# Performance work log

Measured on AMD Instinct MI355X. Metric: run time of the kernel, lower is better.

## Reference

```python
import jax, jax.numpy as jnp
import numpy as np

B = 32          # batch of input networks (INRs)
D = 128         # d_hid
H = 8           # attention heads
DH = D // H
L = 3           # RT layers
DOUT = 10
LAYOUT = [2, 32, 32, 1]          # INR layer layout -> graph nodes
N = 2 + 32 + 32 + 1              # 67 nodes
POS_LAYOUT = [1, 1, 32, 32, 1]   # [1]*layout[0] + layout[1:-1] + [1]*layout[-1]


def _ln(x, g, b, eps=1e-5):
    m = x.mean(-1, keepdims=True)
    v = ((x - m) ** 2).mean(-1, keepdims=True)
    return (x - m) * jax.lax.rsqrt(v + eps) * g + b


def _gelu(x):
    return jax.nn.gelu(x, approximate=False)


def setup_inputs() -> dict:
    key = jax.random.key(0)
    cnt = [0]
    def nk():
        cnt[0] += 1
        return jax.random.fold_in(key, cnt[0])
    def rn(shape, s=0.02):
        return (s * jax.random.normal(nk(), shape)).astype(jnp.float32)
    z = lambda *s: jnp.zeros(s, jnp.float32)
    o = lambda *s: jnp.ones(s, jnp.float32)
    inp = dict(
        w0=rn((B, 2, 32, 1), 1.0), w1=rn((B, 32, 32, 1), 1.0), w2=rn((B, 32, 1, 1), 1.0),
        b0=rn((B, 32, 1), 1.0), b1=rn((B, 32, 1), 1.0), b2=rn((B, 1, 1), 1.0),
        pw_W=rn((1, D)), pw_b=z(D), pb_W=rn((1, D)), pb_b=z(D),
        node_in_W=rn((D, D)), node_in_b=z(D), edge_in_W=rn((D, D)), edge_in_b=z(D),
        pos_embed=rn((len(POS_LAYOUT), D), 1.0),
        aln_g=o(L, D), aln_b=z(L, D),
        Wqkv_n=rn((L, D, 3 * D)), Wqkv_e=rn((L, D, 3 * D)), Wao=rn((L, D, D)), bao=z(L, D),
        Wl0=rn((L, D, D)), bl0=z(L, D),
        nln_g=o(L, D), nln_b=z(L, D),
        nW1=rn((L, D, 2 * D)), nb1=z(L, 2 * D), nW2=rn((L, 2 * D, D)), nb2=z(L, D),
        eln_g=o(L, D), eln_b=z(L, D),
        We=rn((L, 2 * D, D)), be=z(L, D),
        Ws=rn((L, D, D)), bs=z(L, D), Wt=rn((L, D, D)), bt=z(L, D),
        Wer=rn((L, D, D)), Wec=rn((L, D, D)), We1=rn((L, D, D)), be1=z(L, D),
        Wel0=rn((L, D, D)), bel0=z(L, D),
        mln_g=o(L, D), mln_b=z(L, D),
        mW1=rn((L, D, 2 * D)), mb1=z(L, 2 * D), mW2=rn((L, 2 * D, D)), mb2=z(L, D),
        Wo1=rn((D, D)), bo1=z(D), Wo2=rn((D, DOUT)), bo2=z(DOUT),
    )
    return inp


def _forward(w0, w1, w2, b0, b1, b2, pw_W, pw_b, pb_W, pb_b, node_in_W, node_in_b,
             edge_in_W, edge_in_b, pos_embed, aln_g, aln_b, Wqkv_n, Wqkv_e, Wao, bao,
             Wl0, bl0, nln_g, nln_b, nW1, nb1, nW2, nb2, eln_g, eln_b, We, be, Ws, bs,
             Wt, bt, Wer, Wec, We1, be1, Wel0, bel0, mln_g, mln_b, mW1, mb1, mW2, mb2,
             Wo1, bo1, Wo2, bo2):
    # ---- GraphConstructor / batch_to_graphs (layout [2,32,32,1], offsets 0/2/34/66) ----
    nf = jnp.zeros((B, N, 1), w0.dtype)
    ef = jnp.zeros((B, N, N, 1), w0.dtype)
    ef = ef.at[:, 0:2, 2:34].set(w0).at[:, 2:34, 34:66].set(w1).at[:, 34:66, 66:67].set(w2)
    nf = nf.at[:, 2:34].set(b0).at[:, 34:66].set(b1).at[:, 66:67].set(b2)
    node = nf @ pb_W + pb_b            # proj_bias: Linear(1, D)
    edge = ef @ pw_W + pw_b            # proj_weight: Linear(1, D)
    node = node @ node_in_W + node_in_b
    edge = edge @ edge_in_W + edge_in_b
    pos = jnp.concatenate([jnp.broadcast_to(pos_embed[i], (n, D))
                           for i, n in enumerate(POS_LAYOUT)], axis=0)  # [N, D]
    node = node + pos

    scale = 1.0 / np.sqrt(DH)
    for l in range(L):
        # ---- RTAttention (edge-biased multi-head attention) ----
        h = _ln(node, aln_g[l], aln_b[l])
        qkv_n = (h @ Wqkv_n[l]).reshape(B, N, H, 3, DH).transpose(0, 2, 3, 1, 4)       # b H 3 n dh
        qn, kn, vn = qkv_n[:, :, 0], qkv_n[:, :, 1], qkv_n[:, :, 2]
        qkv_e = (edge @ Wqkv_e[l]).reshape(B, N, N, H, 3, DH).transpose(0, 3, 4, 1, 2, 5)  # b H 3 n m dh
        q = qn[:, :, :, None, :] + qkv_e[:, :, 0]
        k = kn[:, :, None, :, :] + qkv_e[:, :, 1]
        v = vn[:, :, None, :, :] + qkv_e[:, :, 2]
        att = jax.nn.softmax((q * k).sum(-1) * scale, axis=-1)                          # b H n m
        o = jnp.einsum('bhnm,bhnmd->bhnd', att, v).transpose(0, 2, 1, 3).reshape(B, N, D)
        node = node + ((o @ Wao[l] + bao[l]) @ Wl0[l] + bl0[l])
        node = node + (_gelu(_ln(node, nln_g[l], nln_b[l]) @ nW1[l] + nb1[l]) @ nW2[l] + nb2[l])
        # ---- Edge update (EdgeMLP with forward/reversed edges + node/row/col terms) ----
        en = _ln(edge, eln_g[l], eln_b[l])
        m = jnp.concatenate([en, en.transpose(0, 2, 1, 3)], axis=-1) @ We[l] + be[l]
        m = m + (node @ Ws[l] + bs[l])[:, :, None, :] + (node @ Wt[l] + bt[l])[:, None, :, :]
        m = m + en.mean(2, keepdims=True) @ Wer[l] + en.mean(1, keepdims=True) @ Wec[l]
        m = _gelu(m) @ We1[l] + be1[l]
        edge = edge + (m @ Wel0[l] + bel0[l])
        edge = edge + (_gelu(_ln(edge, mln_g[l], mln_b[l]) @ mW1[l] + mb1[l]) @ mW2[l] + mb2[l])

    g = node.mean(1)                                        # mean pooling over nodes
    return jax.nn.relu(g @ Wo1 + bo1) @ Wo2 + bo2           # [B, DOUT]


def reference(w0, w1, w2, b0, b1, b2, pw_W, pw_b, pb_W, pb_b, node_in_W, node_in_b,
              edge_in_W, edge_in_b, pos_embed, aln_g, aln_b, Wqkv_n, Wqkv_e, Wao, bao,
              Wl0, bl0, nln_g, nln_b, nW1, nb1, nW2, nb2, eln_g, eln_b, We, be, Ws, bs,
              Wt, bt, Wer, Wec, We1, be1, Wel0, bel0, mln_g, mln_b, mW1, mb1, mW2, mb2,
              Wo1, bo1, Wo2, bo2):
    return _forward(w0, w1, w2, b0, b1, b2, pw_W, pw_b, pb_W, pb_b, node_in_W, node_in_b,
                    edge_in_W, edge_in_b, pos_embed, aln_g, aln_b, Wqkv_n, Wqkv_e, Wao, bao,
                    Wl0, bl0, nln_g, nln_b, nW1, nb1, nW2, nb2, eln_g, eln_b, We, be, Ws, bs,
                    Wt, bt, Wer, Wec, We1, be1, Wel0, bel0, mln_g, mln_b, mW1, mb1, mW2, mb2,
                    Wo1, bo1, Wo2, bo2)
```

## Files before the change

### kernel.cpp

```cpp
#include <hip/hip_runtime.h>
#include <math.h>

constexpr int B_ = 32, N_ = 67, D_ = 128, H_ = 8, DH_ = 16, L_ = 3;
constexpr int NN_ = N_ * N_;
constexpr int RN_ = B_ * N_;
constexpr int RE_ = B_ * NN_;
constexpr int DOUT_ = 10;

typedef __attribute__((ext_vector_type(8))) short short8;
typedef __attribute__((ext_vector_type(4))) float f32x4;

__device__ __forceinline__ float gelu_f(float x) {
  return 0.5f * x * (1.f + erff(x * 0.70710678118654752f));
}
__device__ __forceinline__ ushort f2b(float x) {
  union { float f; unsigned u; } v; v.f = x;
  return (ushort)((v.u + 0x7FFFu + ((v.u >> 16) & 1u)) >> 16);
}
__device__ __forceinline__ float b2f(ushort u) {
  union { unsigned u; float f; } v; v.u = (unsigned)u << 16; return v.f;
}

__global__ void k_comb(const float* __restrict__ Wao, const float* __restrict__ bao,
                       const float* __restrict__ Wl0, const float* __restrict__ bl0,
// ... 79 lines not shown
  node[idx] = nf * vecs[d] + vecs[D_ + d] + pos[pr * D_ + d];
}

__global__ void k_init_edge(const float* __restrict__ w0, const float* __restrict__ w1,
                            const float* __restrict__ w2, const float* __restrict__ vecs,
                            ushort* __restrict__ edge) {
  int idx = blockIdx.x * blockDim.x + threadIdx.x;
  if (idx >= RE_ * D_) return;
  int r = idx >> 7, d = idx & 127;
  int b = r / NN_;
  int rem = r - b * NN_;
  int n = rem / N_, m = rem - n * N_;
  float ef = 0.f;
  if (n < 2)        { if (m >= 2 && m < 34)  ef = w0[(b * 2 + n) * 32 + (m - 2)]; }
  else if (n < 34)  { if (m >= 34 && m < 66) ef = w1[(b * 32 + (n - 2)) * 32 + (m - 34)]; }
  else if (n < 66)  { if (m == 66)           ef = w2[b * 32 + (n - 34)]; }
  edge[idx] = f2b(ef * vecs[2 * D_ + d] + vecs[3 * D_ + d]);
}

__global__ void k_ln(const float* __restrict__ in, float* __restrict__ out,
                     const float* __restrict__ g, const float* __restrict__ b, int R) {
  int row = blockIdx.x * 4 + (threadIdx.x >> 6);
  int lane = threadIdx.x & 63;
  if (row >= R) return;
  const float* x = in + (size_t)row * D_;
  float x0 = x[lane], x1 = x[lane + 64];
  float s = x0 + x1;
  for (int off = 32; off; off >>= 1) s += __shfl_xor(s, off);
  float mean = s * (1.f / 128.f);
  float d0 = x0 - mean, d1 = x1 - mean;
  float v = d0 * d0 + d1 * d1;
  for (int off = 32; off; off >>= 1) v += __shfl_xor(v, off);
  float rstd = rsqrtf(v * (1.f / 128.f) + 1e-5f);
  out[(size_t)row * D_ + lane]      = d0 * rstd * g[lane] + b[lane];
  out[(size_t)row * D_ + lane + 64] = d1 * rstd * g[lane + 64] + b[lane + 64];
}

template <int MODE>
__global__ __launch_bounds__(256) void k_gemm(const float* __restrict__ A, const float* __restrict__ W,
                                              const float* __restrict__ bias, float* __restrict__ out,
                                              int R, int K, int C, int ldw, int ldo) {
  __shared__ float As[16][68];
  __shared__ float Wsh[16][68];
  int r0 = blockIdx.x * 64, c0 = blockIdx.y * 64;
  int tid = threadIdx.x;
  int tr = tid >> 4, tc = tid & 15;
  float acc[4][4] = {};
  for (int kk = 0; kk < K; kk += 16) {
#pragma unroll
    for (int i = 0; i < 4; i++) {
      int lin = tid + i * 256;
      int r_in = lin >> 4, k_in = lin & 15;
      int r = r0 + r_in;
      As[k_in][r_in] = (r < R) ? A[(size_t)r * K + kk + k_in] : 0.f;
    }
#pragma unroll
    for (int i = 0; i < 4; i++) {
      int lin = tid + i * 256;
      int k_in = lin >> 6, c_in = lin & 63;
      int c = c0 + c_in;
      Wsh[k_in][c_in] = (c < C) ? W[(size_t)(kk + k_in) * ldw + c] : 0.f;
    }
    __syncthreads();
#pragma unroll
    for (int k = 0; k < 16; k++) {
      float4 a4 = *reinterpret_cast<const float4*>(&As[k][tr * 4]);
      float4 b4 = *reinterpret_cast<const float4*>(&Wsh[k][tc * 4]);
      float av[4] = {a4.x, a4.y, a4.z, a4.w};
      float bv[4] = {b4.x, b4.y, b4.z, b4.w};
#pragma unroll
      for (int i = 0; i < 4; i++)
#pragma unroll
        for (int j = 0; j < 4; j++) acc[i][j] += av[i] * bv[j];
    }
    __syncthreads();
  }
#pragma unroll
  for (int i = 0; i < 4; i++) {
    int r = r0 + tr * 4 + i;
    if (r >= R) continue;
#pragma unroll
    for (int j = 0; j < 4; j++) {
      int c = c0 + tc * 4 + j;
      if (c >= C) continue;
      float v = acc[i][j] + (bias ? bias[c] : 0.f);
      size_t o = (size_t)r * ldo + c;
      if (MODE == 0) out[o] = v;
      else if (MODE == 1) out[o] = gelu_f(v);
      else out[o] += v;
    }
  }
}

__global__ __launch_bounds__(256) void k_nvec(
    const float* __restrict__ node, const float* __restrict__ rmean, const float* __restrict__ cmean,
    const float* __restrict__ Ws, const float* __restrict__ Wer,
    const float* __restrict__ Wt, const float* __restrict__ Wec,
    const float* __restrict__ bs, const float* __restrict__ be, const float* __restrict__ bt,
    float* __restrict__ rvec, float* __restrict__ cvec) {
  __shared__ float Ash[16][68];
  __shared__ float Wsh[16][68];
  int which = blockIdx.z;
  const float* A2 = which ? cmean : rmean;
  const float* W1 = which ? Wt : Ws;
  const float* W2 = which ? Wec : Wer;
  float* out = which ? cvec : rvec;
  int r0 = blockIdx.x * 64, c0 = blockIdx.y * 64;
  int tid = threadIdx.x, tr = tid >> 4, tc = tid & 15;
  float acc[4][4] = {};
  for (int kk = 0; kk < 256; kk += 16) {
#pragma unroll
    for (int i = 0; i < 4; i++) {
      int lin = tid + i * 256;
      int r_in = lin >> 4, k_in = lin & 15;
      int r = r0 + r_in, k = kk + k_in;
      float v = 0.f;
      if (r < RN_) v = (k < 128) ? node[(size_t)r * 128 + k] : A2[(size_t)r * 128 + (k - 128)];
      Ash[k_in][r_in] = v;
    }
#pragma unroll
    for (int i = 0; i < 4; i++) {
      int lin = tid + i * 256;
      int k_in = lin >> 6, c_in = lin & 63;
      int k = kk + k_in, c = c0 + c_in;
      Wsh[k_in][c_in] = (k < 128) ? W1[(size_t)k * 128 + c] : W2[(size_t)(k - 128) * 128 + c];
    }
    __syncthreads();
#pragma unroll
    for (int k = 0; k < 16; k++) {
      float4 a4 = *reinterpret_cast<const float4*>(&Ash[k][tr * 4]);
      float4 b4 = *reinterpret_cast<const float4*>(&Wsh[k][tc * 4]);
      float av[4] = {a4.x, a4.y, a4.z, a4.w};
      float bv[4] = {b4.x, b4.y, b4.z, b4.w};
#pragma unroll
      for (int i = 0; i < 4; i++)
#pragma unroll
        for (int j = 0; j < 4; j++) acc[i][j] += av[i] * bv[j];
    }
    __syncthreads();
  }
#pragma unroll
  for (int i = 0; i < 4; i++) {
    int r = r0 + tr * 4 + i;
    if (r >= RN_) continue;
#pragma unroll
    for (int j = 0; j < 4; j++) {
      int c = c0 + tc * 4 + j;
      float bias = which ? bt[c] : (bs[c] + be[c]);
      out[(size_t)r * 128 + c] = acc[i][j] + bias;
    }
  }
}

__global__ __launch_bounds__(256, 3) void k_eattn(
    const ushort* __restrict__ edge, const float* __restrict__ qkvn,
    const ushort* __restrict__ wqf,
    const float* __restrict__ gE, const float* __restrict__ bE,
    float* __restrict__ stats, float* __restrict__ rmean,
    float* __restrict__ obuf) {
  __shared__ __align__(16) ushort ed[68 * 128];
  __shared__ __align__(16) ushort Eb[68 * 202];
  __shared__ float qn_s[384];
  __shared__ float sc[4][68];
  __shared__ float red[4][16][4];
  __shared__ float stmu[68], strs[68];
  int bn = blockIdx.x;
  int b = bn / N_;
  int tid = threadIdx.x;
  int w = tid >> 6, lane = tid & 63, lr = lane & 15, lk8 = (lane >> 4) * 8;
  int swz = (lr & 7) << 3;
  int rb = (lane >> 4) * 4;
  size_t ebase = (size_t)bn * N_ * 128;

  for (int i = 0; i < 5; i++) {
    int u = tid + i * 256;
    if (u < 67 * 16) {
      int row = u >> 4, k8 = (u & 15) * 8;
      short8 t = __builtin_nontemporal_load(
          reinterpret_cast<const short8*>(&edge[ebase + (size_t)row * 128 + k8]));
      *reinterpret_cast<short8*>(&ed[row * 128 + (k8 ^ ((row & 7) << 3))]) = t;
      float s = 0.f, q = 0.f;
#pragma unroll
      for (int j = 0; j < 8; j++) { float v = b2f((ushort)t[j]); s += v; q += v * v; }
      for (int o = 8; o; o >>= 1) { s += __shfl_xor(s, o); q += __shfl_xor(q, o); }
      if ((u & 15) == 0) {
        float mu = s * (1.f / 128.f);
        float rs = rsqrtf(q * (1.f / 128.f) - mu * mu + 1e-5f);
        stmu[row] = mu; strs[row] = rs;
        stats[2 * (size_t)(bn * N_ + row)] = mu;
        stats[2 * (size_t)(bn * N_ + row) + 1] = rs;
      }
    }
  }
  for (int i = tid; i < 384; i += 256) qn_s[i] = qkvn[(size_t)bn * 384 + i];
  __syncthreads();
  if (tid < 128) {
    float s = 0.f;
    for (int m = 0; m < 67; m++)
      s += (b2f(ed[m * 128 + (tid ^ ((m & 7) << 3))]) - stmu[m]) * strs[m];
    rmean[(size_t)bn * 128 + tid] = gE[tid] * (s * (1.f / 67.f)) + bE[tid];
  }

  for (int ch = 0; ch < 2; ch++) {
    int h0 = ch * 4;
    f32x4 acc[5][3] = {};
#pragma unroll
    for (int ks = 0; ks < 4; ks++) {
      int kof = ks * 32 + lk8;
      short8 af[5];
#pragma unroll
      for (int rf = 0; rf < 5; rf++)
        af[rf] = *reinterpret_cast<const short8*>(&ed[(rf * 16 + lr) * 128 + (kof ^ swz)]);
#pragma unroll
      for (int cl = 0; cl < 3; cl++) {
        short8 bf = *reinterpret_cast<const short8*>(
            &wqf[(size_t)(((ch * 12 + w * 3 + cl) * 4 + ks) * 64 + lane) * 8]);
#pragma unroll
        for (int rf = 0; rf < 5; rf++)
          acc[rf][cl] = __builtin_amdgcn_mfma_f32_16x16x32_bf16(af[rf], bf, acc[rf][cl], 0, 0, 0);
      }
    }
#pragma unroll
    for (int rf = 0; rf < 5; rf++)
#pragma unroll
      for (int cl = 0; cl < 3; cl++) {
        int colc = (w * 3 + cl) * 16 + lr;
#pragma unroll
        for (int rg = 0; rg < 4; rg++) {
          int er = rf * 16 + rb + rg;
          if (er < 67) Eb[er * 202 + colc] = f2b(acc[rf][cl][rg]);
        }
      }
    __syncthreads();
    for (int idx = tid; idx < 268; idx += 256) {
      int h2 = idx / 67, m = idx - h2 * 67;
      const ushort* e = &Eb[m * 202 + h2 * 48];
      const float* kn = &qkvn[(size_t)(b * N_ + m) * 384 + (h0 + h2) * 48 + 16];
      const float* qn = &qn_s[(h0 + h2) * 48];
      float s2 = 0.f;
#pragma unroll
      for (int d = 0; d < 16; d++)
        s2 += (qn[d] + b2f(e[d])) * (kn[d] + b2f(e[16 + d]));
      sc[h2][m] = s2 * 0.25f;
    }
    __syncthreads();
    {
      float v0 = (lane < 67) ? sc[w][lane] : -1e30f;
      float v1 = (lane < 3) ? sc[w][lane + 64] : -1e30f;
      float mx = fmaxf(v0, v1);
      for (int o = 32; o; o >>= 1) mx = fmaxf(mx, __shfl_xor(mx, o));
      float e0 = (lane < 67) ? expf(v0 - mx) : 0.f;
      float e1 = (lane < 3) ? expf(v1 - mx) : 0.f;
      float ss = e0 + e1;
      for (int o = 32; o; o >>= 1) ss += __shfl_xor(ss, o);
      float inv = 1.f / ss;
      if (lane < 67) sc[w][lane] = e0 * inv;
      if (lane < 3) sc[w][lane + 64] = e1 * inv;
    }
    __syncthreads();
    {
      int item = tid >> 2, c = tid & 3;
      int h2 = item >> 4, d = item & 15;
      float p = 0.f;
      for (int m = c; m < 67; m += 4) {
        float v = qkvn[(size_t)(b * N_ + m) * 384 + (h0 + h2) * 48 + 32 + d]
                + b2f(Eb[m * 202 + h2 * 48 + 32 + d]);
        p += sc[h2][m] * v;
      }
      red[h2][d][c] = p;
    }
    __syncthreads();
    if (tid < 64) {
      int h2 = tid >> 4, d = tid & 15;
      obuf[(size_t)bn * 128 + (h0 + h2) * 16 + d] =
          red[h2][d][0] + red[h2][d][1] + red[h2][d][2] + red[h2][d][3];
    }
    __syncthreads();
  }
}

__global__ void k_colmean(const ushort* __restrict__ edge, const float* __restrict__ stats,
                          const float* __restrict__ g, const float* __restrict__ bb,
                          float* __restrict__ cmean) {
  int bm = blockIdx.x;
  int b = bm / N_, m = bm - b * N_;
  int d = threadIdx.x;
  float s = 0.f;
  for (int n = 0; n < N_; n++) {
    size_t r = (size_t)b * NN_ + (size_t)n * N_ + m;
    s += (b2f(edge[r * D_ + d]) - stats[2 * r]) * stats[2 * r + 1];
  }
  cmean[(size_t)bm * D_ + d] = g[d] * (s * (1.f / 67.f)) + bb[d];
}

__global__ __launch_bounds__(256, 2) void k_fedge(
    const ushort* __restrict__ ein, ushort* __restrict__ eout,
    const float* __restrict__ stats,
    const float* __restrict__ gE, const float* __restrict__ bE,
    const ushort* __restrict__ wef,
    const float* __restrict__ rvec, const float* __restrict__ cvec,
    const ushort* __restrict__ wcef,
    const float* __restrict__ bcE,
    const float* __restrict__ gM, const float* __restrict__ bM,
    const ushort* __restrict__ w1f,
    const float* __restrict__ mb1,
    const ushort* __restrict__ w2f,
    const float* __restrict__ mb2) {
  __shared__ __align__(16) ushort As[64 * 256];
  __shared__ __align__(16) ushort mt[64 * 128];
  __shared__ __align__(16) ushort Wb[32 * 512];
  int tid = threadIdx.x;
  int r0 = blockIdx.x * 64;
  int w = tid >> 6, lane = tid & 63, lr = lane & 15, lk8 = (lane >> 4) * 8;
  int swz = (lr & 7) << 3;
  int rb = (lane >> 4) * 4;
  int arow = w * 16 + lr;

  auto stageW = [&](const ushort* src) {
#pragma unroll
    for (int i = 0; i < 8; i++) {
      int u = tid + i * 256;
      short8 t = *reinterpret_cast<const short8*>(&src[(size_t)u * 8]);
      *reinterpret_cast<short8*>(&Wb[u * 8]) = t;
    }
  };

#pragma unroll
  for (int i = 0; i < 8; i++) {
    int u = tid + i * 256;
    int row = u >> 5, c8 = (u & 31) * 8;
    int gr = r0 + row;
    int grc = (gr < RE_) ? gr : 0;
    int cc = c8 & 127;
    short8 t;
    float mu, rs;
    if (c8 < 128) {
      size_t srow = (size_t)grc;
      mu = stats[2 * srow]; rs = stats[2 * srow + 1];
      t = *reinterpret_cast<const short8*>(&ein[srow * 128 + cc]);
    } else {
      int b = grc / NN_; int rem = grc - b * NN_;
      int n = rem / N_, m = rem - n * N_;
      size_t srow = (size_t)b * NN_ + (size_t)m * N_ + n;
      mu = stats[2 * srow]; rs = stats[2 * srow + 1];
      t = __builtin_nontemporal_load(reinterpret_cast<const short8*>(&ein[srow * 128 + cc]));
    }
    short8 r8;
#pragma unroll
    for (int j = 0; j < 8; j++) {
      float v = (b2f((ushort)t[j]) - mu) * rs * gE[cc + j] + bE[cc + j];
      r8[j] = (short)f2b(v);
    }
    *reinterpret_cast<short8*>(&As[row * 256 + (c8 ^ ((row & 7) << 3))]) = r8;
  }
  int rvb[4], cvb[4], grows[4]; bool vr[4];
#pragma unroll
  for (int rg = 0; rg < 4; rg++) {
    int gr = r0 + w * 16 + rb + rg;
    vr[rg] = gr < RE_;
    int grc = vr[rg] ? gr : 0;
    grows[rg] = grc;
    int b = grc / NN_; int rem = grc - b * NN_;
    int n = rem / N_, m = rem - n * N_;
    rvb[rg] = (b * N_ + n) * 128;
    cvb[rg] = (b * N_ + m) * 128;
  }
  __syncthreads();

  for (int h = 0; h < 2; h++) {
    if (h) __syncthreads();
    stageW(wef + (size_t)h * 32 * 512);
    __syncthreads();
    f32x4 acc[4] = {};
#pragma unroll
    for (int ks = 0; ks < 8; ks++) {
      int kof = ks * 32 + lk8;
      short8 af = *reinterpret_cast<const short8*>(&As[arow * 256 + (kof ^ swz)]);
#pragma unroll
      for (int cf = 0; cf < 4; cf++) {
        short8 bf = *reinterpret_cast<const short8*>(&Wb[(cf * 8 + ks) * 512 + lane * 8]);
        acc[cf] = __builtin_amdgcn_mfma_f32_16x16x32_bf16(af, bf, acc[cf], 0, 0, 0);
      }
    }
#pragma unroll
    for (int cf = 0; cf < 4; cf++) {
      int c = (h * 4 + cf) * 16 + lr;
#pragma unroll
      for (int rg = 0; rg < 4; rg++) {
        float v = acc[cf][rg] + rvec[rvb[rg] + c] + cvec[cvb[rg] + c];
        int mrow = w * 16 + rb + rg;
        mt[mrow * 128 + (c ^ ((mrow & 7) << 3))] = f2b(gelu_f(v));
      }
    }
  }

  __syncthreads();
  stageW(wcef);
  __syncthreads();
  f32x4 e1[8] = {};
#pragma unroll
  for (int ks = 0; ks < 4; ks++) {
    int kof = ks * 32 + lk8;
    short8 af = *reinterpret_cast<const short8*>(&mt[arow * 128 + (kof ^ swz)]);
#pragma unroll
    for (int cf = 0; cf < 8; cf++) {
      short8 bf = *reinterpret_cast<const short8*>(&Wb[(cf * 4 + ks) * 512 + lane * 8]);
      e1[cf] = __builtin_amdgcn_mfma_f32_16x16x32_bf16(af, bf, e1[cf], 0, 0, 0);
    }
  }
  float mu_[4], rs_[4];
  {
    float sr[4] = {0, 0, 0, 0}, qr[4] = {0, 0, 0, 0};
#pragma unroll
    for (int cf = 0; cf < 8; cf++) {
      int c = cf * 16 + lr;
#pragma unroll
      for (int rg = 0; rg < 4; rg++) {
        float v = e1[cf][rg] + bcE[c] + b2f(ein[(size_t)grows[rg] * 128 + c]);
        e1[cf][rg] = v;
        sr[rg] += v; qr[rg] += v * v;
      }
    }
#pragma unroll
    for (int rg = 0; rg < 4; rg++) {
      float s = sr[rg], q = qr[rg];
      for (int o = 8; o; o >>= 1) { s += __shfl_xor(s, o); q += __shfl_xor(q, o); }
      mu_[rg] = s * (1.f / 128.f);
      rs_[rg] = rsqrtf(q * (1.f / 128.f) - mu_[rg] * mu_[rg] + 1e-5f);
    }
  }
#pragma unroll
  for (int cf = 0; cf < 8; cf++) {
    int c = cf * 16 + lr;
#pragma unroll
    for (int rg = 0; rg < 4; rg++) {
      int mrow = w * 16 + rb + rg;
      mt[mrow * 128 + (c ^ ((mrow & 7) << 3))] =
          f2b((e1[cf][rg] - mu_[rg]) * rs_[rg] * gM[c] + bM[c]);
    }
  }

  for (int h = 0; h < 2; h++) {
    __syncthreads();
    stageW(w1f + (size_t)h * 32 * 512);
    __syncthreads();
    f32x4 acc[8] = {};
#pragma unroll
    for (int ks = 0; ks < 4; ks++) {
      int kof = ks * 32 + lk8;
      short8 af = *reinterpret_cast<const short8*>(&mt[arow * 128 + (kof ^ swz)]);
#pragma unroll
      for (int cf = 0; cf < 8; cf++) {
        short8 bf = *reinterpret_cast<const short8*>(&Wb[(cf * 4 + ks) * 512 + lane * 8]);
        acc[cf] = __builtin_amdgcn_mfma_f32_16x16x32_bf16(af, bf, acc[cf], 0, 0, 0);
      }
    }
#pragma unroll
    for (int cf = 0; cf < 8; cf++) {
      int c2 = (h * 8 + cf) * 16 + lr;
#pragma unroll
      for (int rg = 0; rg < 4; rg++) {
        int mrow = w * 16 + rb + rg;
        As[mrow * 256 + (c2 ^ ((mrow & 7) << 3))] = f2b(gelu_f(acc[cf][rg] + mb1[c2]));
      }
    }
  }

  for (int h = 0; h < 2; h++) {
    __syncthreads();
    stageW(w2f + (size_t)h * 32 * 512);
    __syncthreads();
    f32x4 acc[4] = {};
#pragma unroll
    for (int ks = 0; ks < 8; ks++) {
      int kof = ks * 32 + lk8;
      short8 af = *reinterpret_cast<const short8*>(&As[arow * 256 + (kof ^ swz)]);
#pragma unroll
      for (int cf = 0; cf < 4; cf++) {
        short8 bf = *reinterpret_cast<const short8*>(&Wb[(cf * 8 + ks) * 512 + lane * 8]);
        acc[cf] = __builtin_amdgcn_mfma_f32_16x16x32_bf16(af, bf, acc[cf], 0, 0, 0);
      }
    }
#pragma unroll
    for (int cf = 0; cf < 4; cf++) {
      int cg = h * 4 + cf;
      int c = cg * 16 + lr;
#pragma unroll
      for (int rg = 0; rg < 4; rg++) {
        int mrow = w * 16 + rb + rg;
        mt[mrow * 128 + (c ^ ((mrow & 7) << 3))] = f2b(e1[cg][rg] + acc[cf][rg] + mb2[c]);
      }
    }
  }

  __syncthreads();
#pragma unroll
  for (int p = 0; p < 4; p++) {
    int u = p * 256 + tid;
    int row = u >> 4, col8 = (u & 15) * 8;
    int gr = r0 + row;
    if (gr < RE_) {
      short8 v = *reinterpret_cast<const short8*>(&mt[row * 128 + (col8 ^ ((row & 7) << 3))]);
      __builtin_nontemporal_store(v, reinterpret_cast<short8*>(&eout[(size_t)gr * 128 + col8]));
    }
  }
}

__global__ void k_head(const float* __restrict__ node, const float* __restrict__ Wo1,
                       const float* __restrict__ bo1, const float* __restrict__ Wo2,
                       const float* __restrict__ bo2, float* __restrict__ out) {
  int b = blockIdx.x;
  int tid = threadIdx.x;
  __shared__ float gsh[D_];
  __shared__ float h1[D_];
  float s = 0.f;
  for (int n = 0; n < N_; n++) s += node[((size_t)b * N_ + n) * D_ + tid];
  gsh[tid] = s * (1.f / 67.f);
  __syncthreads();
  float a = 0.f;
  for (int k = 0; k < D_; k++) a += gsh[k] * Wo1[k * D_ + tid];
  h1[tid] = fmaxf(a + bo1[tid], 0.f);
  __syncthreads();
  if (tid < DOUT_) {
    float r = 0.f;
    for (int k = 0; k < D_; k++) r += h1[k] * Wo2[k * DOUT_ + tid];
    out[b * DOUT_ + tid] = r + bo2[tid];
  }
}

extern "C" void kernel_launch(void* const* d_in, const int* in_sizes, int n_in,
                              void* d_out, int out_size, void* d_ws, size_t ws_size,
                              hipStream_t stream) {
  const float* w0   = (const float*)d_in[0];
  const float* w1   = (const float*)d_in[1];
  const float* w2   = (const float*)d_in[2];
  const float* b0   = (const float*)d_in[3];
  const float* b1   = (const float*)d_in[4];
  const float* b2   = (const float*)d_in[5];
  const float* pwW  = (const float*)d_in[6];
  const float* pwb  = (const float*)d_in[7];
  const float* pbW  = (const float*)d_in[8];
  const float* pbb  = (const float*)d_in[9];
  const float* niW  = (const float*)d_in[10];
  const float* nib  = (const float*)d_in[11];
  const float* eiW  = (const float*)d_in[12];
  const float* eib  = (const float*)d_in[13];
  const float* pos  = (const float*)d_in[14];
  const float* alng = (const float*)d_in[15];
  const float* alnb = (const float*)d_in[16];
  const float* Wqkvn= (const float*)d_in[17];
  const float* Wqkve= (const float*)d_in[18];
  const float* Wao  = (const float*)d_in[19];
  const float* bao  = (const float*)d_in[20];
  const float* Wl0  = (const float*)d_in[21];
  const float* bl0  = (const float*)d_in[22];
  const float* nlng = (const float*)d_in[23];
  const float* nlnb = (const float*)d_in[24];
  const float* nW1  = (const float*)d_in[25];
  const float* nb1  = (const float*)d_in[26];
  const float* nW2  = (const float*)d_in[27];
  const float* nb2  = (const float*)d_in[28];
  const float* elng = (const float*)d_in[29];
  const float* elnb = (const float*)d_in[30];
  const float* We   = (const float*)d_in[31];
  const float* be   = (const float*)d_in[32];
  const float* Ws   = (const float*)d_in[33];
  const float* bs   = (const float*)d_in[34];
  const float* Wt   = (const float*)d_in[35];
  const float* bt   = (const float*)d_in[36];
  const float* Wer  = (const float*)d_in[37];
  const float* Wec  = (const float*)d_in[38];
  const float* We1  = (const float*)d_in[39];
  const float* be1  = (const float*)d_in[40];
  const float* Wel0 = (const float*)d_in[41];
  const float* bel0 = (const float*)d_in[42];
  const float* mlng = (const float*)d_in[43];
  const float* mlnb = (const float*)d_in[44];
  const float* mW1  = (const float*)d_in[45];
  const float* mb1  = (const float*)d_in[46];
  const float* mW2  = (const float*)d_in[47];
  const float* mb2  = (const float*)d_in[48];
  const float* Wo1  = (const float*)d_in[49];
  const float* bo1  = (const float*)d_in[50];
  const float* Wo2  = (const float*)d_in[51];
  const float* bo2  = (const float*)d_in[52];
  float* outp = (float*)d_out;

  const size_t E = (size_t)RE_ * D_;
  const size_t NODE = (size_t)RN_ * D_;
  const int DD = D_ * D_;

  float* ws = (float*)d_ws;
  size_t off = 0;
  auto alloc = [&](size_t nf) { float* p = ws + off; off += nf; return p; };
  ushort* edgeA = (ushort*)alloc(E / 2);
  ushort* edgeB = (ushort*)alloc(E / 2);
  float* stats = alloc(2 * (size_t)RE_);
  float* node  = alloc(NODE);
  float* h_ln  = alloc(NODE);
  float* qkvn  = alloc(3 * NODE);
  float* obuf  = alloc(NODE);
  float* t_n   = alloc(2 * NODE);
  float* rmean = alloc(NODE);
  float* cmean = alloc(NODE);
  float* rvec  = alloc(NODE);
  float* cvec  = alloc(NODE);
  float* WcN   = alloc((size_t)L_ * DD);
  float* bcN   = alloc((size_t)L_ * D_);
  float* WcE   = alloc((size_t)L_ * DD);
  float* bcE   = alloc((size_t)L_ * D_);
  float* vecs  = alloc(4 * D_);
  ushort* wbf   = (ushort*)alloc(245760);
  ushort* wq_fm = wbf;
  ushort* we_fm = wq_fm + (size_t)L_ * 49152;
  ushort* wce_fm= we_fm + (size_t)L_ * 32768;
  ushort* w1_fm = wce_fm + (size_t)L_ * 16384;
  ushort* w2_fm = w1_fm + (size_t)L_ * 32768;
  (void)ws_size; (void)in_sizes; (void)n_in; (void)out_size;

  k_comb<<<(2 * L_ * DD + 255) / 256, 256, 0, stream>>>(Wao, bao, Wl0, bl0, We1, be1, Wel0, bel0,
                                                        WcN, bcN, WcE, bcE);
  k_prepw<<<1920, 256, 0, stream>>>(Wqkve, We, WcE, mW1, mW2, wq_fm, we_fm, wce_fm, w1_fm, w2_fm);
  k_vecs<<<1, 128, 0, stream>>>(pbW, pbb, niW, nib, pwW, pwb, eiW, eib, vecs);
  k_init_node<<<(RN_ * D_ + 255) / 256, 256, 0, stream>>>(b0, b1, b2, vecs, pos, node);
  k_init_edge<<<(int)((E + 255) / 256), 256, 0, stream>>>(w0, w1, w2, vecs, edgeA);

  const int GE = (RE_ + 63) / 64;
  const int GN = (RN_ + 63) / 64;
  const int GSN = (RN_ + 3) / 4;

  for (int l = 0; l < L_; l++) {
    ushort* ein  = (l & 1) ? edgeB : edgeA;
    ushort* eout = (l & 1) ? edgeA : edgeB;
    const float* Wqn = Wqkvn + (size_t)l * D_ * 384;

    k_ln<<<GSN, 256, 0, stream>>>(node, h_ln, alng + l * D_, alnb + l * D_, RN_);
    k_gemm<0><<<dim3(GN, 6), 256, 0, stream>>>(h_ln, Wqn, nullptr, qkvn, RN_, 128, 384, 384, 384);
    k_eattn<<<RN_, 256, 0, stream>>>(ein, qkvn, wq_fm + (size_t)l * 49152,
                                     elng + l * D_, elnb + l * D_, stats, rmean, obuf);
    k_gemm<2><<<dim3(GN, 2), 256, 0, stream>>>(obuf, WcN + (size_t)l * DD, bcN + l * D_, node,
                                               RN_, 128, 128, 128, 128);

    k_ln<<<GSN, 256, 0, stream>>>(node, h_ln, nlng + l * D_, nlnb + l * D_, RN_);
    k_gemm<1><<<dim3(GN, 4), 256, 0, stream>>>(h_ln, nW1 + (size_t)l * D_ * 256, nb1 + l * 256, t_n,
                                               RN_, 128, 256, 256, 256);
    k_gemm<2><<<dim3(GN, 2), 256, 0, stream>>>(t_n, nW2 + (size_t)l * 256 * D_, nb2 + l * D_, node,
                                               RN_, 256, 128, 128, 128);

    k_colmean<<<RN_, 128, 0, stream>>>(ein, stats, elng + l * D_, elnb + l * D_, cmean);
    k_nvec<<<dim3(GN, 2, 2), 256, 0, stream>>>(node, rmean, cmean,
                                               Ws + (size_t)l * DD, Wer + (size_t)l * DD,
                                               Wt + (size_t)l * DD, Wec + (size_t)l * DD,
                                               bs + l * D_, be + l * D_, bt + l * D_,
                                               rvec, cvec);

// ... 12 lines not shown
```

Before: 1.209 ms.

## Double-buffer weight chunks via registers in fused edge kernel, raise occupancy

Replaces the monolithic 32KB weight staging in k_fedge with 16KB chunks held in a two-slot shared buffer. Each next chunk is prefetched into registers while MFMAs run on the current one, then written to the other slot. This halves the weight buffer and overlaps global loads with compute, and both edge kernels now request 4 blocks per CU through launch bounds. The catch is more barriers and extra register pressure from the staging registers and full 8-fragment accumulators, which could spill under the tighter launch-bound limit.

```diff
diff --git a/kernel.cpp b/kernel.cpp
--- a/kernel.cpp
+++ b/kernel.cpp
@@ -255,7 +255,7 @@
   }
 }
 
-__global__ __launch_bounds__(256, 3) void k_eattn(
+__global__ __launch_bounds__(256, 4) void k_eattn(
     const ushort* __restrict__ edge, const float* __restrict__ qkvn,
     const ushort* __restrict__ wqf,
     const float* __restrict__ gE, const float* __restrict__ bE,
@@ -396,7 +396,7 @@
   cmean[(size_t)bm * D_ + d] = g[d] * (s * (1.f / 67.f)) + bb[d];
 }
 
-__global__ __launch_bounds__(256, 2) void k_fedge(
+__global__ __launch_bounds__(256, 4) void k_fedge(
     const ushort* __restrict__ ein, ushort* __restrict__ eout,
     const float* __restrict__ stats,
     const float* __restrict__ gE, const float* __restrict__ bE,
@@ -411,7 +411,7 @@
     const float* __restrict__ mb2) {
   __shared__ __align__(16) ushort As[64 * 256];
   __shared__ __align__(16) ushort mt[64 * 128];
-  __shared__ __align__(16) ushort Wb[32 * 512];
+  __shared__ __align__(16) ushort Wb[2][16 * 512];
   int tid = threadIdx.x;
   int r0 = blockIdx.x * 64;
   int w = tid >> 6, lane = tid & 63, lr = lane & 15, lk8 = (lane >> 4) * 8;
@@ -419,15 +419,25 @@
   int rb = (lane >> 4) * 4;
   int arow = w * 16 + lr;
 
-  auto stageW = [&](const ushort* src) {
-#pragma unroll
-    for (int i = 0; i < 8; i++) {
-      int u = tid + i * 256;
-      short8 t = *reinterpret_cast<const short8*>(&src[(size_t)u * 8]);
-      *reinterpret_cast<short8*>(&Wb[u * 8]) = t;
+  short8 stg[4];
+  auto LOADC = [&](const ushort* blob, int cf0, int ks0, int nks) {
+#pragma unroll
+    for (int i = 0; i < 4; i++) {
+      int idx = tid + i * 256;
+      int fl = idx >> 6, pos = idx & 63;
+      int g = (cf0 + (fl >> 2)) * nks + ks0 + (fl & 3);
+      stg[i] = *reinterpret_cast<const short8*>(&blob[(size_t)(g * 64 + pos) * 8]);
     }
   };
-
+  auto WRITEC = [&](int buf) {
+#pragma unroll
+    for (int i = 0; i < 4; i++) {
+      int idx = tid + i * 256;
+      *reinterpret_cast<short8*>(&Wb[buf][idx * 8]) = stg[i];
+    }
+  };
+
+  LOADC(wef, 0, 0, 8);
 #pragma unroll
   for (int i = 0; i < 8; i++) {
     int u = tid + i * 256;
@@ -468,50 +478,66 @@
     rvb[rg] = (b * N_ + n) * 128;
     cvb[rg] = (b * N_ + m) * 128;
   }
+  WRITEC(0);
   __syncthreads();
 
-  for (int h = 0; h < 2; h++) {
-    if (h) __syncthreads();
-    stageW(wef + (size_t)h * 32 * 512);
-    __syncthreads();
-    f32x4 acc[4] = {};
-#pragma unroll
-    for (int ks = 0; ks < 8; ks++) {
-      int kof = ks * 32 + lk8;
+  f32x4 acc1[8] = {};
+  auto p1c = [&](int cfg, int ksg, int buf) {
+#pragma unroll
+    for (int ksl = 0; ksl < 4; ksl++) {
+      int kof = (ksg * 4 + ksl) * 32 + lk8;
       short8 af = *reinterpret_cast<const short8*>(&As[arow * 256 + (kof ^ swz)]);
 #pragma unroll
-      for (int cf = 0; cf < 4; cf++) {
-        short8 bf = *reinterpret_cast<const short8*>(&Wb[(cf * 8 + ks) * 512 + lane * 8]);
-        acc[cf] = __builtin_amdgcn_mfma_f32_16x16x32_bf16(af, bf, acc[cf], 0, 0, 0);
-      }
-    }
-#pragma unroll
-    for (int cf = 0; cf < 4; cf++) {
-      int c = (h * 4 + cf) * 16 + lr;
-#pragma unroll
-      for (int rg = 0; rg < 4; rg++) {
-        float v = acc[cf][rg] + rvec[rvb[rg] + c] + cvec[cvb[rg] + c];
-        int mrow = w * 16 + rb + rg;
-        mt[mrow * 128 + (c ^ ((mrow & 7) << 3))] = f2b(gelu_f(v));
-      }
-    }
-  }
-
-  __syncthreads();
-  stageW(wcef);
-  __syncthreads();
+      for (int cfl = 0; cfl < 4; cfl++) {
+        short8 bf = *reinterpret_cast<const short8*>(&Wb[buf][(cfl * 4 + ksl) * 512 + lane * 8]);
+        acc1[cfg * 4 + cfl] =
+            __builtin_amdgcn_mfma_f32_16x16x32_bf16(af, bf, acc1[cfg * 4 + cfl], 0, 0, 0);
+      }
+    }
+  };
+
+  LOADC(wef, 4, 0, 8);
+  p1c(0, 0, 0);
+  WRITEC(1); __syncthreads();
+  LOADC(wef, 0, 4, 8);
+  p1c(1, 0, 1);
+  WRITEC(0); __syncthreads();
+  LOADC(wef, 4, 4, 8);
+  p1c(0, 1, 0);
+  WRITEC(1); __syncthreads();
+  LOADC(wcef, 0, 0, 4);
+  p1c(1, 1, 1);
+#pragma unroll
+  for (int cf = 0; cf < 8; cf++) {
+    int c = cf * 16 + lr;
+#pragma unroll
+    for (int rg = 0; rg < 4; rg++) {
+      float v = acc1[cf][rg] + rvec[rvb[rg] + c] + cvec[cvb[rg] + c];
+      int mrow = w * 16 + rb + rg;
+      mt[mrow * 128 + (c ^ ((mrow & 7) << 3))] = f2b(gelu_f(v));
+    }
+  }
+  WRITEC(0); __syncthreads();
+
   f32x4 e1[8] = {};
-#pragma unroll
-  for (int ks = 0; ks < 4; ks++) {
-    int kof = ks * 32 + lk8;
-    short8 af = *reinterpret_cast<const short8*>(&mt[arow * 128 + (kof ^ swz)]);
-#pragma unroll
-    for (int cf = 0; cf < 8; cf++) {
-      short8 bf = *reinterpret_cast<const short8*>(&Wb[(cf * 4 + ks) * 512 + lane * 8]);
-      e1[cf] = __builtin_amdgcn_mfma_f32_16x16x32_bf16(af, bf, e1[cf], 0, 0, 0);
-    }
-  }
-  float mu_[4], rs_[4];
+  auto p2c = [&](int cfg, int buf) {
+#pragma unroll
+    for (int ksl = 0; ksl < 4; ksl++) {
+      int kof = ksl * 32 + lk8;
+      short8 af = *reinterpret_cast<const short8*>(&mt[arow * 128 + (kof ^ swz)]);
+#pragma unroll
+      for (int cfl = 0; cfl < 4; cfl++) {
+        short8 bf = *reinterpret_cast<const short8*>(&Wb[buf][(cfl * 4 + ksl) * 512 + lane * 8]);
+        e1[cfg * 4 + cfl] =
+            __builtin_amdgcn_mfma_f32_16x16x32_bf16(af, bf, e1[cfg * 4 + cfl], 0, 0, 0);
+      }
+    }
+  };
+  LOADC(wcef, 4, 0, 4);
+  p2c(0, 0);
+  WRITEC(1); __syncthreads();
+  LOADC(w1f, 0, 0, 4);
+  p2c(1, 1);
   {
     float sr[4] = {0, 0, 0, 0}, qr[4] = {0, 0, 0, 0};
 #pragma unroll
@@ -528,74 +554,88 @@
     for (int rg = 0; rg < 4; rg++) {
       float s = sr[rg], q = qr[rg];
       for (int o = 8; o; o >>= 1) { s += __shfl_xor(s, o); q += __shfl_xor(q, o); }
-      mu_[rg] = s * (1.f / 128.f);
-      rs_[rg] = rsqrtf(q * (1.f / 128.f) - mu_[rg] * mu_[rg] + 1e-5f);
-    }
-  }
+      float mu = s * (1.f / 128.f);
+      float rs = rsqrtf(q * (1.f / 128.f) - mu * mu + 1e-5f);
+#pragma unroll
+      for (int cf = 0; cf < 8; cf++) {
+        int c = cf * 16 + lr;
+        int mrow = w * 16 + rb + rg;
+        mt[mrow * 128 + (c ^ ((mrow & 7) << 3))] =
+            f2b((e1[cf][rg] - mu) * rs * gM[c] + bM[c]);
+      }
+    }
+  }
+  WRITEC(0); __syncthreads();
+
+  auto p4c = [&](int q, int buf) {
+    f32x4 a4[4] = {};
+#pragma unroll
+    for (int ksl = 0; ksl < 4; ksl++) {
+      int kof = ksl * 32 + lk8;
+      short8 af = *reinterpret_cast<const short8*>(&mt[arow * 128 + (kof ^ swz)]);
+#pragma unroll
+      for (int cfl = 0; cfl < 4; cfl++) {
+        short8 bf = *reinterpret_cast<const short8*>(&Wb[buf][(cfl * 4 + ksl) * 512 + lane * 8]);
+        a4[cfl] = __builtin_amdgcn_mfma_f32_16x16x32_bf16(af, bf, a4[cfl], 0, 0, 0);
+      }
+    }
+#pragma unroll
+    for (int cfl = 0; cfl < 4; cfl++) {
+      int c2 = (q * 4 + cfl) * 16 + lr;
+#pragma unroll
+      for (int rg = 0; rg < 4; rg++) {
+        int mrow = w * 16 + rb + rg;
+        As[mrow * 256 + (c2 ^ ((mrow & 7) << 3))] = f2b(gelu_f(a4[cfl][rg] + mb1[c2]));
+      }
+    }
+  };
+  LOADC(w1f, 4, 0, 4);
+  p4c(0, 0);
+  WRITEC(1); __syncthreads();
+  LOADC(w1f, 8, 0, 4);
+  p4c(1, 1);
+  WRITEC(0); __syncthreads();
+  LOADC(w1f, 12, 0, 4);
+  p4c(2, 0);
+  WRITEC(1); __syncthreads();
+  LOADC(w2f, 0, 0, 8);
+  p4c(3, 1);
+  WRITEC(0); __syncthreads();
+
+  f32x4 acc5[8] = {};
+  auto p5c = [&](int cfg, int ksg, int buf) {
+#pragma unroll
+    for (int ksl = 0; ksl < 4; ksl++) {
+      int kof = (ksg * 4 + ksl) * 32 + lk8;
+      short8 af = *reinterpret_cast<const short8*>(&As[arow * 256 + (kof ^ swz)]);
+#pragma unroll
+      for (int cfl = 0; cfl < 4; cfl++) {
+        short8 bf = *reinterpret_cast<const short8*>(&Wb[buf][(cfl * 4 + ksl) * 512 + lane * 8]);
+        acc5[cfg * 4 + cfl] =
+            __builtin_amdgcn_mfma_f32_16x16x32_bf16(af, bf, acc5[cfg * 4 + cfl], 0, 0, 0);
+      }
+    }
+  };
+  LOADC(w2f, 4, 0, 8);
+  p5c(0, 0, 0);
+  WRITEC(1); __syncthreads();
+  LOADC(w2f, 0, 4, 8);
+  p5c(1, 0, 1);
+  WRITEC(0); __syncthreads();
+  LOADC(w2f, 4, 4, 8);
+  p5c(0, 1, 0);
+  WRITEC(1); __syncthreads();
+  p5c(1, 1, 1);
+
 #pragma unroll
   for (int cf = 0; cf < 8; cf++) {
     int c = cf * 16 + lr;
 #pragma unroll
     for (int rg = 0; rg < 4; rg++) {
       int mrow = w * 16 + rb + rg;
-      mt[mrow * 128 + (c ^ ((mrow & 7) << 3))] =
-          f2b((e1[cf][rg] - mu_[rg]) * rs_[rg] * gM[c] + bM[c]);
-    }
-  }
-
-  for (int h = 0; h < 2; h++) {
-    __syncthreads();
-    stageW(w1f + (size_t)h * 32 * 512);
-    __syncthreads();
-    f32x4 acc[8] = {};
-#pragma unroll
-    for (int ks = 0; ks < 4; ks++) {
-      int kof = ks * 32 + lk8;
-      short8 af = *reinterpret_cast<const short8*>(&mt[arow * 128 + (kof ^ swz)]);
-#pragma unroll
-      for (int cf = 0; cf < 8; cf++) {
-        short8 bf = *reinterpret_cast<const short8*>(&Wb[(cf * 4 + ks) * 512 + lane * 8]);
-        acc[cf] = __builtin_amdgcn_mfma_f32_16x16x32_bf16(af, bf, acc[cf], 0, 0, 0);
-      }
-    }
-#pragma unroll
-    for (int cf = 0; cf < 8; cf++) {
-      int c2 = (h * 8 + cf) * 16 + lr;
-#pragma unroll
-      for (int rg = 0; rg < 4; rg++) {
-        int mrow = w * 16 + rb + rg;
-        As[mrow * 256 + (c2 ^ ((mrow & 7) << 3))] = f2b(gelu_f(acc[cf][rg] + mb1[c2]));
-      }
-    }
-  }
-
-  for (int h = 0; h < 2; h++) {
-    __syncthreads();
-    stageW(w2f + (size_t)h * 32 * 512);
-    __syncthreads();
-    f32x4 acc[4] = {};
-#pragma unroll
-    for (int ks = 0; ks < 8; ks++) {
-      int kof = ks * 32 + lk8;
-      short8 af = *reinterpret_cast<const short8*>(&As[arow * 256 + (kof ^ swz)]);
-#pragma unroll
-      for (int cf = 0; cf < 4; cf++) {
-        short8 bf = *reinterpret_cast<const short8*>(&Wb[(cf * 8 + ks) * 512 + lane * 8]);
-        acc[cf] = __builtin_amdgcn_mfma_f32_16x16x32_bf16(af, bf, acc[cf], 0, 0, 0);
-      }
-    }
-#pragma unroll
-    for (int cf = 0; cf < 4; cf++) {
-      int cg = h * 4 + cf;
-      int c = cg * 16 + lr;
-#pragma unroll
-      for (int rg = 0; rg < 4; rg++) {
-        int mrow = w * 16 + rb + rg;
-        mt[mrow * 128 + (c ^ ((mrow & 7) << 3))] = f2b(e1[cg][rg] + acc[cf][rg] + mb2[c]);
-      }
-    }
-  }
-
+      mt[mrow * 128 + (c ^ ((mrow & 7) << 3))] = f2b(e1[cf][rg] + acc5[cf][rg] + mb2[c]);
+    }
+  }
   __syncthreads();
 #pragma unroll
   for (int p = 0; p < 4; p++) {
```

After: 1.736 ms. 43.6% more time.

## Shrink k_fedge shared memory by keeping A fragments in registers and split MLP

Applied to the files above, without the earlier changes.

The fused edge kernel no longer stages the normalized 256-wide input tile in LDS. Each lane loads and normalizes its own A fragments straight into registers. The edge MLP hidden layer is processed in two 128-column halves, each accumulating directly into the second GEMM's output, so the 64x256 hidden buffer is gone and one 64x128 scratch tile is reused throughout. This cuts LDS per block from 80KB to 48KB so launch bounds can request 3 blocks per CU, and k_eattn's bound is raised to 4. The cost is higher register pressure from the held fragments and accumulators, which could cause spills, plus extra barriers and weight restaging.

```diff
diff --git a/kernel.cpp b/kernel.cpp
--- a/kernel.cpp
+++ b/kernel.cpp
@@ -255,7 +255,7 @@
   }
 }
 
-__global__ __launch_bounds__(256, 3) void k_eattn(
+__global__ __launch_bounds__(256, 4) void k_eattn(
     const ushort* __restrict__ edge, const float* __restrict__ qkvn,
     const ushort* __restrict__ wqf,
     const float* __restrict__ gE, const float* __restrict__ bE,
@@ -396,7 +396,7 @@
   cmean[(size_t)bm * D_ + d] = g[d] * (s * (1.f / 67.f)) + bb[d];
 }
 
-__global__ __launch_bounds__(256, 2) void k_fedge(
+__global__ __launch_bounds__(256, 3) void k_fedge(
     const ushort* __restrict__ ein, ushort* __restrict__ eout,
     const float* __restrict__ stats,
     const float* __restrict__ gE, const float* __restrict__ bE,
@@ -409,9 +409,8 @@
     const float* __restrict__ mb1,
     const ushort* __restrict__ w2f,
     const float* __restrict__ mb2) {
-  __shared__ __align__(16) ushort As[64 * 256];
-  __shared__ __align__(16) ushort mt[64 * 128];
   __shared__ __align__(16) ushort Wb[32 * 512];
+  __shared__ __align__(16) ushort scp[64 * 128];
   int tid = threadIdx.x;
   int r0 = blockIdx.x * 64;
   int w = tid >> 6, lane = tid & 63, lr = lane & 15, lk8 = (lane >> 4) * 8;
@@ -419,42 +418,49 @@
   int rb = (lane >> 4) * 4;
   int arow = w * 16 + lr;
 
-  auto stageW = [&](const ushort* src) {
+  int gro = r0 + arow;
+  int groc = (gro < RE_) ? gro : 0;
+  int bo = groc / NN_; int remo = groc - bo * NN_;
+  int no = remo / N_, mo = remo - no * N_;
+  size_t srow_o = (size_t)groc;
+  size_t srow_t = (size_t)bo * NN_ + (size_t)mo * N_ + no;
+  float mu_o = stats[2 * srow_o], rs_o = stats[2 * srow_o + 1];
+  float mu_t = stats[2 * srow_t], rs_t = stats[2 * srow_t + 1];
+
+  auto stageLin = [&](const ushort* src) {
 #pragma unroll
     for (int i = 0; i < 8; i++) {
       int u = tid + i * 256;
-      short8 t = *reinterpret_cast<const short8*>(&src[(size_t)u * 8]);
-      *reinterpret_cast<short8*>(&Wb[u * 8]) = t;
+      *reinterpret_cast<short8*>(&Wb[u * 8]) =
+          *reinterpret_cast<const short8*>(&src[(size_t)u * 8]);
     }
   };
-
-#pragma unroll
-  for (int i = 0; i < 8; i++) {
-    int u = tid + i * 256;
-    int row = u >> 5, c8 = (u & 31) * 8;
-    int gr = r0 + row;
-    int grc = (gr < RE_) ? gr : 0;
-    int cc = c8 & 127;
-    short8 t;
-    float mu, rs;
-    if (c8 < 128) {
-      size_t srow = (size_t)grc;
-      mu = stats[2 * srow]; rs = stats[2 * srow + 1];
-      t = *reinterpret_cast<const short8*>(&ein[srow * 128 + cc]);
-    } else {
-      int b = grc / NN_; int rem = grc - b * NN_;
-      int n = rem / N_, m = rem - n * N_;
-      size_t srow = (size_t)b * NN_ + (size_t)m * N_ + n;
-      mu = stats[2 * srow]; rs = stats[2 * srow + 1];
-      t = __builtin_nontemporal_load(reinterpret_cast<const short8*>(&ein[srow * 128 + cc]));
-    }
+  auto stageW2 = [&](const ushort* blob, int ks0) {
+#pragma unroll
+    for (int i = 0; i < 8; i++) {
+      int u = tid + i * 256;
+      int fl = u >> 6, pos = u & 63;
+      int g = (fl >> 2) * 8 + ks0 + (fl & 3);
+      *reinterpret_cast<short8*>(&Wb[(fl * 64 + pos) * 8]) =
+          *reinterpret_cast<const short8*>(&blob[(size_t)(g * 64 + pos) * 8]);
+    }
+  };
+
+  short8 af[8];
+#pragma unroll
+  for (int ks = 0; ks < 8; ks++) {
+    bool own = ks < 4;
+    size_t sr = own ? srow_o : srow_t;
+    int kc = (own ? ks : ks - 4) * 32 + lk8;
+    short8 t = *reinterpret_cast<const short8*>(&ein[sr * 128 + kc]);
+    float mu = own ? mu_o : mu_t, rs = own ? rs_o : rs_t;
     short8 r8;
 #pragma unroll
     for (int j = 0; j < 8; j++) {
-      float v = (b2f((ushort)t[j]) - mu) * rs * gE[cc + j] + bE[cc + j];
+      float v = (b2f((ushort)t[j]) - mu) * rs * gE[kc + j] + bE[kc + j];
       r8[j] = (short)f2b(v);
     }
-    *reinterpret_cast<short8*>(&As[row * 256 + (c8 ^ ((row & 7) << 3))]) = r8;
+    af[ks] = r8;
   }
   int rvb[4], cvb[4], grows[4]; bool vr[4];
 #pragma unroll
@@ -463,55 +469,58 @@
     vr[rg] = gr < RE_;
     int grc = vr[rg] ? gr : 0;
     grows[rg] = grc;
-    int b = grc / NN_; int rem = grc - b * NN_;
-    int n = rem / N_, m = rem - n * N_;
-    rvb[rg] = (b * N_ + n) * 128;
-    cvb[rg] = (b * N_ + m) * 128;
-  }
-  __syncthreads();
-
-  for (int h = 0; h < 2; h++) {
-    if (h) __syncthreads();
-    stageW(wef + (size_t)h * 32 * 512);
-    __syncthreads();
-    f32x4 acc[4] = {};
-#pragma unroll
-    for (int ks = 0; ks < 8; ks++) {
-      int kof = ks * 32 + lk8;
-      short8 af = *reinterpret_cast<const short8*>(&As[arow * 256 + (kof ^ swz)]);
-#pragma unroll
-      for (int cf = 0; cf < 4; cf++) {
-        short8 bf = *reinterpret_cast<const short8*>(&Wb[(cf * 8 + ks) * 512 + lane * 8]);
-        acc[cf] = __builtin_amdgcn_mfma_f32_16x16x32_bf16(af, bf, acc[cf], 0, 0, 0);
-      }
-    }
-#pragma unroll
-    for (int cf = 0; cf < 4; cf++) {
-      int c = (h * 4 + cf) * 16 + lr;
-#pragma unroll
-      for (int rg = 0; rg < 4; rg++) {
-        float v = acc[cf][rg] + rvec[rvb[rg] + c] + cvec[cvb[rg] + c];
-        int mrow = w * 16 + rb + rg;
-        mt[mrow * 128 + (c ^ ((mrow & 7) << 3))] = f2b(gelu_f(v));
-      }
-    }
-  }
-
-  __syncthreads();
-  stageW(wcef);
+    int b2 = grc / NN_; int rem = grc - b2 * NN_;
+    int n2 = rem / N_, m2 = rem - n2 * N_;
+    rvb[rg] = (b2 * N_ + n2) * 128;
+    cvb[rg] = (b2 * N_ + m2) * 128;
+  }
+
+  f32x4 acc1[8] = {};
+  stageLin(wef);
+  __syncthreads();
+#pragma unroll
+  for (int ks = 0; ks < 8; ks++)
+#pragma unroll
+    for (int cf = 0; cf < 4; cf++)
+      acc1[cf] = __builtin_amdgcn_mfma_f32_16x16x32_bf16(
+          af[ks], *reinterpret_cast<const short8*>(&Wb[(cf * 8 + ks) * 512 + lane * 8]),
+          acc1[cf], 0, 0, 0);
+  __syncthreads();
+  stageLin(wef + 32 * 512);
+  __syncthreads();
+#pragma unroll
+  for (int ks = 0; ks < 8; ks++)
+#pragma unroll
+    for (int cf = 0; cf < 4; cf++)
+      acc1[4 + cf] = __builtin_amdgcn_mfma_f32_16x16x32_bf16(
+          af[ks], *reinterpret_cast<const short8*>(&Wb[(cf * 8 + ks) * 512 + lane * 8]),
+          acc1[4 + cf], 0, 0, 0);
+#pragma unroll
+  for (int cf = 0; cf < 8; cf++) {
+    int c = cf * 16 + lr;
+#pragma unroll
+    for (int rg = 0; rg < 4; rg++) {
+      float v = acc1[cf][rg] + rvec[rvb[rg] + c] + cvec[cvb[rg] + c];
+      int mrow = w * 16 + rb + rg;
+      scp[mrow * 128 + (c ^ ((mrow & 7) << 3))] = f2b(gelu_f(v));
+    }
+  }
+  short8 mtf[4];
+#pragma unroll
+  for (int ks = 0; ks < 4; ks++)
+    mtf[ks] = *reinterpret_cast<const short8*>(&scp[arow * 128 + ((ks * 32 + lk8) ^ swz)]);
+
+  __syncthreads();
+  stageLin(wcef);
   __syncthreads();
   f32x4 e1[8] = {};
 #pragma unroll
-  for (int ks = 0; ks < 4; ks++) {
-    int kof = ks * 32 + lk8;
-    short8 af = *reinterpret_cast<const short8*>(&mt[arow * 128 + (kof ^ swz)]);
-#pragma unroll
-    for (int cf = 0; cf < 8; cf++) {
-      short8 bf = *reinterpret_cast<const short8*>(&Wb[(cf * 4 + ks) * 512 + lane * 8]);
-      e1[cf] = __builtin_amdgcn_mfma_f32_16x16x32_bf16(af, bf, e1[cf], 0, 0, 0);
-    }
-  }
-  float mu_[4], rs_[4];
+  for (int ks = 0; ks < 4; ks++)
+#pragma unroll
+    for (int cf = 0; cf < 8; cf++)
+      e1[cf] = __builtin_amdgcn_mfma_f32_16x16x32_bf16(
+          mtf[ks], *reinterpret_cast<const short8*>(&Wb[(cf * 4 + ks) * 512 + lane * 8]),
+          e1[cf], 0, 0, 0);
   {
     float sr[4] = {0, 0, 0, 0}, qr[4] = {0, 0, 0, 0};
 #pragma unroll
@@ -528,74 +537,70 @@
     for (int rg = 0; rg < 4; rg++) {
       float s = sr[rg], q = qr[rg];
       for (int o = 8; o; o >>= 1) { s += __shfl_xor(s, o); q += __shfl_xor(q, o); }
-      mu_[rg] = s * (1.f / 128.f);
-      rs_[rg] = rsqrtf(q * (1.f / 128.f) - mu_[rg] * mu_[rg] + 1e-5f);
-    }
-  }
+      float mu = s * (1.f / 128.f);
+      float rs = rsqrtf(q * (1.f / 128.f) - mu * mu + 1e-5f);
+#pragma unroll
+      for (int cf = 0; cf < 8; cf++) {
+        int c = cf * 16 + lr;
+        int mrow = w * 16 + rb + rg;
+        scp[mrow * 128 + (c ^ ((mrow & 7) << 3))] =
+            f2b((e1[cf][rg] - mu) * rs * gM[c] + bM[c]);
+      }
+    }
+  }
+#pragma unroll
+  for (int ks = 0; ks < 4; ks++)
+    mtf[ks] = *reinterpret_cast<const short8*>(&scp[arow * 128 + ((ks * 32 + lk8) ^ swz)]);
+
+  f32x4 acc5[8] = {};
+#pragma unroll 1
+  for (int h = 0; h < 2; h++) {
+    __syncthreads();
+    stageLin(w1f + (size_t)h * 32 * 512);
+    __syncthreads();
+    f32x4 a4[8] = {};
+#pragma unroll
+    for (int ks = 0; ks < 4; ks++)
+#pragma unroll
+      for (int cf = 0; cf < 8; cf++)
+        a4[cf] = __builtin_amdgcn_mfma_f32_16x16x32_bf16(
+            mtf[ks], *reinterpret_cast<const short8*>(&Wb[(cf * 4 + ks) * 512 + lane * 8]),
+            a4[cf], 0, 0, 0);
+#pragma unroll
+    for (int cf = 0; cf < 8; cf++) {
+      int c2 = (h * 8 + cf) * 16 + lr;
+      int cl = cf * 16 + lr;
+#pragma unroll
+      for (int rg = 0; rg < 4; rg++) {
+        int mrow = w * 16 + rb + rg;
+        scp[mrow * 128 + (cl ^ ((mrow & 7) << 3))] = f2b(gelu_f(a4[cf][rg] + mb1[c2]));
+      }
+    }
+    __syncthreads();
+    stageW2(w2f, h * 4);
+    __syncthreads();
+    short8 hhf;
+#pragma unroll
+    for (int ks = 0; ks < 4; ks++) {
+      hhf = *reinterpret_cast<const short8*>(&scp[arow * 128 + ((ks * 32 + lk8) ^ swz)]);
+#pragma unroll
+      for (int cf = 0; cf < 8; cf++)
+        acc5[cf] = __builtin_amdgcn_mfma_f32_16x16x32_bf16(
+            hhf, *reinterpret_cast<const short8*>(&Wb[(cf * 4 + ks) * 512 + lane * 8]),
+            acc5[cf], 0, 0, 0);
+    }
+  }
+
+  __syncthreads();
 #pragma unroll
   for (int cf = 0; cf < 8; cf++) {
     int c = cf * 16 + lr;
 #pragma unroll
     for (int rg = 0; rg < 4; rg++) {
       int mrow = w * 16 + rb + rg;
-      mt[mrow * 128 + (c ^ ((mrow & 7) << 3))] =
-          f2b((e1[cf][rg] - mu_[rg]) * rs_[rg] * gM[c] + bM[c]);
-    }
-  }
-
-  for (int h = 0; h < 2; h++) {
-    __syncthreads();
-    stageW(w1f + (size_t)h * 32 * 512);
-    __syncthreads();
-    f32x4 acc[8] = {};
-#pragma unroll
-    for (int ks = 0; ks < 4; ks++) {
-      int kof = ks * 32 + lk8;
-      short8 af = *reinterpret_cast<const short8*>(&mt[arow * 128 + (kof ^ swz)]);
-#pragma unroll
-      for (int cf = 0; cf < 8; cf++) {
-        short8 bf = *reinterpret_cast<const short8*>(&Wb[(cf * 4 + ks) * 512 + lane * 8]);
-        acc[cf] = __builtin_amdgcn_mfma_f32_16x16x32_bf16(af, bf, acc[cf], 0, 0, 0);
-      }
-    }
-#pragma unroll
-    for (int cf = 0; cf < 8; cf++) {
-      int c2 = (h * 8 + cf) * 16 + lr;
-#pragma unroll
-      for (int rg = 0; rg < 4; rg++) {
-        int mrow = w * 16 + rb + rg;
-        As[mrow * 256 + (c2 ^ ((mrow & 7) << 3))] = f2b(gelu_f(acc[cf][rg] + mb1[c2]));
-      }
-    }
-  }
-
-  for (int h = 0; h < 2; h++) {
-    __syncthreads();
-    stageW(w2f + (size_t)h * 32 * 512);
-    __syncthreads();
-    f32x4 acc[4] = {};
-#pragma unroll
-    for (int ks = 0; ks < 8; ks++) {
-      int kof = ks * 32 + lk8;
-      short8 af = *reinterpret_cast<const short8*>(&As[arow * 256 + (kof ^ swz)]);
-#pragma unroll
-      for (int cf = 0; cf < 4; cf++) {
-        short8 bf = *reinterpret_cast<const short8*>(&Wb[(cf * 8 + ks) * 512 + lane * 8]);
-        acc[cf] = __builtin_amdgcn_mfma_f32_16x16x32_bf16(af, bf, acc[cf], 0, 0, 0);
-      }
-    }
-#pragma unroll
-    for (int cf = 0; cf < 4; cf++) {
-      int cg = h * 4 + cf;
-      int c = cg * 16 + lr;
-#pragma unroll
-      for (int rg = 0; rg < 4; rg++) {
-        int mrow = w * 16 + rb + rg;
-        mt[mrow * 128 + (c ^ ((mrow & 7) << 3))] = f2b(e1[cg][rg] + acc[cf][rg] + mb2[c]);
-      }
-    }
-  }
-
+      scp[mrow * 128 + (c ^ ((mrow & 7) << 3))] = f2b(e1[cf][rg] + acc5[cf][rg] + mb2[c]);
+    }
+  }
   __syncthreads();
 #pragma unroll
   for (int p = 0; p < 4; p++) {
@@ -603,7 +608,7 @@
     int row = u >> 4, col8 = (u & 15) * 8;
     int gr = r0 + row;
     if (gr < RE_) {
-      short8 v = *reinterpret_cast<const short8*>(&mt[row * 128 + (col8 ^ ((row & 7) << 3))]);
+      short8 v = *reinterpret_cast<const short8*>(&scp[row * 128 + (col8 ^ ((row & 7) << 3))]);
       __builtin_nontemporal_store(v, reinterpret_cast<short8*>(&eout[(size_t)gr * 128 + col8]));
     }
   }
```

Result: slower. 1.367 ms (+13.1%).
